# Kernel optimization log

Measured on AMD Instinct MI355X. Metric: run time of the kernel, lower is better.

## Reference

```python
import jax, jax.numpy as jnp
import numpy as np

MASK_THR = 0.2
EPS = 1e-12  # torch F.normalize eps


def setup_inputs() -> dict:
    key = jax.random.key(0)
    k1, k2, k3 = jax.random.split(key, 3)
    B, Cin, H, W = 2, 384, 96, 96
    features = jax.random.normal(k1, (B, Cin, H, W), dtype=jnp.float32)
    # projector: Conv2d(384,256,1) -> ReLU -> Conv2d(256,128,1); 1x1 convs == per-pixel GEMMs
    W1 = jax.random.normal(k2, (256, Cin), dtype=jnp.float32) * (1.0 / np.sqrt(Cin))
    b1 = jnp.zeros((256,), dtype=jnp.float32)
    W2 = jax.random.normal(k3, (128, 256), dtype=jnp.float32) * (1.0 / np.sqrt(256))
    b2 = jnp.zeros((128,), dtype=jnp.float32)
    return {"features": features, "W1": W1, "b1": b1, "W2": W2, "b2": b2}


def reference(features, W1, b1, W2, b2):
    B, _, H, Wd = features.shape
    # projector (1x1 convs as channel GEMMs)
    h = jax.nn.relu(jnp.einsum('oc,bchw->bohw', W1, features) + b1[None, :, None, None])
    feat = jnp.einsum('oc,bchw->bohw', W2, h) + b2[None, :, None, None]  # [B,128,H,W]
    # get_mask: L2-normalize over channels, full pairwise similarity, top-2 NN, distance, threshold
    norm = jnp.sqrt(jnp.sum(feat * feat, axis=1, keepdims=True))
    nf = feat / jnp.maximum(norm, EPS)
    C = nf.shape[1]
    rf = jnp.transpose(nf, (0, 2, 3, 1)).reshape(B, H * Wd, C)         # [B,N,C]
    sim = jnp.einsum('bnc,bmc->bnm', rf, rf)                           # [B,N,N]
    _, top2_idx = jax.lax.top_k(sim, 2)
    nn_idx = top2_idx[:, :, 1]                                         # nearest non-self neighbor
    nearest = jnp.take_along_axis(rf, nn_idx[:, :, None], axis=1)      # [B,N,C]
    diff = rf - nearest
    distance = jnp.sqrt(jnp.sum(diff * diff, axis=-1))                 # [B,N]
    mask = (distance > MASK_THR).astype(feat.dtype).reshape(B, 1, H, Wd)
    return mask, distance
```

## Files before the change

### kernel.cpp

```cpp
#include <hip/hip_runtime.h>

#define NHW 9216
#define NB 2
#define NCHUNK 16

typedef short s8v __attribute__((ext_vector_type(8)));
typedef _Float16 h8v __attribute__((ext_vector_type(8)));
typedef float f4v __attribute__((ext_vector_type(4)));
typedef unsigned int u32;
typedef unsigned short u16;

__device__ inline u16 f2bf(float x) {
    u32 u = __float_as_uint(x);
    u += 0x7fffu + ((u >> 16) & 1u);
    return (u16)(u >> 16);
}
__device__ inline u16 f2h(float x) {
    _Float16 h = (_Float16)x;
    return *(u16*)&h;
}

__global__ __launch_bounds__(256) void k_xsplit(const float* __restrict__ X,
                                                u16* __restrict__ xh)
{
    __shared__ float fs[64][65];
    const int tid = threadIdx.x;
    const int b = blockIdx.z, p0 = blockIdx.x * 64, half = blockIdx.y;
    const size_t fb = (size_t)b * 384 * NHW;
    const int px = tid >> 2, sub = tid & 3;
    const size_t g = (size_t)b * NHW + p0 + px;
    for (int pass = half * 3; pass < half * 3 + 3; ++pass) {
        int c0p = pass * 64;
        __syncthreads();
#pragma unroll
        for (int r = 0; r < 16; ++r) {
            int e = r * 256 + tid;
            int cc = e >> 6, p = e & 63;
            fs[cc][p] = X[fb + (size_t)(c0p + cc) * NHW + p0 + p];
        }
        __syncthreads();
        u16 hb[16];
#pragma unroll
        for (int i = 0; i < 16; ++i) hb[i] = f2h(fs[sub * 16 + i][px]);
        size_t o = g * 384 + c0p + sub * 16;
        *(s8v*)&xh[o]     = *(s8v*)&hb[0];
        *(s8v*)&xh[o + 8] = *(s8v*)&hb[8];
    }
}

__global__ __launch_bounds__(256) void k_wsplit(const float* __restrict__ W1,
                                                const float* __restrict__ W2,
                                                u16* __restrict__ w1h, u16* __restrict__ w1l,
                                                u16* __restrict__ w2h)
{
    int i = blockIdx.x * 256 + threadIdx.x;
    if (i < 98304) {
        float v = W1[i];
        _Float16 h = (_Float16)v;
        w1h[i] = *(u16*)&h;
        w1l[i] = f2h(v - (float)h);
    } else {
        int j = i - 98304;
        w2h[j] = f2h(W2[j]);
    }
}

__global__ __launch_bounds__(256, 4) void k_gemm1(const u16* __restrict__ xh,
                                                  const u16* __restrict__ w1h, const u16* __restrict__ w1l,
                                                  const float* __restrict__ b1,
                                                  u16* __restrict__ hh)
{
    union __align__(16) SM {
        struct { u16 B[2][16][512]; } stg;
        u16 bounce[128 * 66];
    };
    __shared__ SM sm;
    const int tid = threadIdx.x;
    const int wave = tid >> 6, l = tid & 63, l15 = l & 15, q = l >> 4;
    const int bx = blockIdx.x;
    const int xcd = bx & 7, k = bx >> 3;
    const int g0 = (xcd * 18 + (k >> 2)) * 128;
    const int c0 = (k & 3) * 64;
    const int gw = g0 + wave * 32;

    auto stage = [&](int kt, int buf) {
#pragma unroll
        for (int r = 0; r < 4; ++r) {
            int cid = r * 4 + wave;
            int spl = cid >> 3, kf = (cid >> 2) & 1, cs = cid & 3;
            const u16* src = (spl ? w1l : w1h) + (size_t)(c0 + cs * 16 + l15) * 384 + kt + kf * 32 + q * 8;
            __builtin_amdgcn_global_load_lds(
                (const __attribute__((address_space(1))) void*)src,
                (__attribute__((address_space(3))) void*)&sm.stg.B[buf][cid][0],
                16, 0, 0);
        }
    };

    f4v acc[2][4];
#pragma unroll
    for (int s = 0; s < 2; ++s)
#pragma unroll
        for (int c = 0; c < 4; ++c) acc[s][c] = (f4v){0.f, 0.f, 0.f, 0.f};

    stage(0, 0);
    __syncthreads();
    for (int t = 0; t < 6; ++t) {
        const int kt = t * 64;
        const int buf = t & 1;
        if (t < 5) stage(kt + 64, buf ^ 1);
        s8v ah[2][2];
#pragma unroll
        for (int s = 0; s < 2; ++s)
#pragma unroll
            for (int kf = 0; kf < 2; ++kf)
                ah[s][kf] = *(const s8v*)&xh[(size_t)(gw + s * 16 + l15) * 384 + kt + kf * 32 + q * 8];
#pragma unroll
        for (int kf = 0; kf < 2; ++kf)
#pragma unroll
            for (int cs = 0; cs < 4; ++cs) {
                s8v bh = *(const s8v*)&sm.stg.B[buf][kf * 4 + cs][l * 8];
                s8v bl = *(const s8v*)&sm.stg.B[buf][8 + kf * 4 + cs][l * 8];
#pragma unroll
                for (int s = 0; s < 2; ++s) {
                    acc[s][cs] = __builtin_amdgcn_mfma_f32_16x16x32_f16(*(h8v*)&ah[s][kf], *(h8v*)&bh, acc[s][cs], 0, 0, 0);
                    acc[s][cs] = __builtin_amdgcn_mfma_f32_16x16x32_f16(*(h8v*)&ah[s][kf], *(h8v*)&bl, acc[s][cs], 0, 0, 0);
                }
            }
        __syncthreads();
    }

#pragma unroll
    for (int s = 0; s < 2; ++s)
#pragma unroll
        for (int cs = 0; cs < 4; ++cs) {
            int c = cs * 16 + l15;
            float bv = b1[c0 + c];
#pragma unroll
            for (int r = 0; r < 4; ++r) {
                int px = wave * 32 + s * 16 + q * 4 + r;
                sm.bounce[px * 66 + c] = f2h(fmaxf(acc[s][cs][r] + bv, 0.f));
            }
        }
    __syncthreads();
    {
        int px = tid >> 1, half = tid & 1;
        u32 tmp[16];
#pragma unroll
        for (int j = 0; j < 16; ++j)
            tmp[j] = *(const u32*)&sm.bounce[px * 66 + half * 32 + j * 2];
        size_t o = (size_t)(g0 + px) * 256 + c0 + half * 32;
#pragma unroll
        for (int j = 0; j < 4; ++j)
            *(s8v*)&hh[o + j * 8] = ((s8v*)tmp)[j];
    }
}

__global__ __launch_bounds__(256) void k_gemm2n(const u16* __restrict__ hh,
                                                const u16* __restrict__ w2h,
                                                const float* __restrict__ b2,
                                                float* __restrict__ rf,
                                                u16* __restrict__ hib)
{
    __shared__ u16 Bs[64][512];
    const int tid = threadIdx.x;
    const int wave = tid >> 6, l = tid & 63, l15 = l & 15, q = l >> 4;
    const int bx = blockIdx.x;
    const int xcd = bx & 7, k = bx >> 3;
    const int g0 = (xcd * 36 + k) * 64;

#pragma unroll
    for (int r = 0; r < 16; ++r) {
        int cid = r * 4 + wave;
        int kf = cid >> 3, cst = cid & 7;
        const u16* src = w2h + (size_t)(cst * 16 + l15) * 256 + kf * 32 + q * 8;
        __builtin_amdgcn_global_load_lds(
            (const __attribute__((address_space(1))) void*)src,
            (__attribute__((address_space(3))) void*)&Bs[cid][0],
            16, 0, 0);
    }
    __syncthreads();

    const int gw = g0 + wave * 16;
    f4v acc[8];
#pragma unroll
    for (int c = 0; c < 8; ++c) acc[c] = (f4v){0.f, 0.f, 0.f, 0.f};

#pragma unroll
    for (int kf = 0; kf < 8; ++kf) {
        s8v ah = *(const s8v*)&hh[(size_t)(gw + l15) * 256 + kf * 32 + q * 8];
#pragma unroll
        for (int cst = 0; cst < 8; ++cst) {
            s8v bh = *(const s8v*)&Bs[kf * 8 + cst][l * 8];
            acc[cst] = __builtin_amdgcn_mfma_f32_16x16x32_f16(*(h8v*)&ah, *(h8v*)&bh, acc[cst], 0, 0, 0);
        }
    }

    float ssq[4] = {0.f, 0.f, 0.f, 0.f};
#pragma unroll
    for (int cst = 0; cst < 8; ++cst) {
        float bv = b2[cst * 16 + l15];
#pragma unroll
        for (int r = 0; r < 4; ++r) {
            acc[cst][r] += bv;
            ssq[r] += acc[cst][r] * acc[cst][r];
        }
    }
#pragma unroll
    for (int r = 0; r < 4; ++r) {
        ssq[r] += __shfl_xor(ssq[r], 1, 64);
        ssq[r] += __shfl_xor(ssq[r], 2, 64);
        ssq[r] += __shfl_xor(ssq[r], 4, 64);
        ssq[r] += __shfl_xor(ssq[r], 8, 64);
        ssq[r] = 1.0f / fmaxf(sqrtf(ssq[r]), 1e-12f);
    }
#pragma unroll
    for (int cst = 0; cst < 8; ++cst)
#pragma unroll
        for (int r = 0; r < 4; ++r) {
            float val = acc[cst][r] * ssq[r];
            size_t o = (size_t)(gw + q * 4 + r) * 128 + cst * 16 + l15;
            rf[o]  = val;
            hib[o] = f2bf(val);
        }
}

__global__ __launch_bounds__(256, 3) void k_simtop(const u16* __restrict__ hi,
                                                   int* __restrict__ cidx)
{
    __shared__ u16 Bs[2][16][512];
    const int tid  = threadIdx.x;
    const int wave = tid >> 6, l = tid & 63, l15 = l & 15, q = l >> 4;
    const int b     = blockIdx.z;
    const int rbase = blockIdx.x * 192;
    const int chunk = blockIdx.y;
    const int cbase = chunk * 576;
    const size_t base = (size_t)b * NHW;
    const int wr0 = rbase + wave * 48;

    s8v ah[3][4];
#pragma unroll
    for (int s = 0; s < 3; ++s) {
        int row = wr0 + s * 16 + l15;
#pragma unroll
        for (int kf = 0; kf < 4; ++kf)
            ah[s][kf] = *(const s8v*)&hi[(base + row) * 128 + kf * 32 + q * 8];
    }

    auto stage = [&](int colt, int buf) {
#pragma unroll
        for (int r = 0; r < 4; ++r) {
            int cid = r * 4 + wave;
            int kf = cid >> 2, cs = cid & 3;
            int col = colt + cs * 16 + l15;
            const u16* src = hi + (base + col) * 128 + kf * 32 + q * 8;
            __builtin_amdgcn_global_load_lds(
                (const __attribute__((address_space(1))) void*)src,
                (__attribute__((address_space(3))) void*)&Bs[buf][cid][0],
                16, 0, 0);
        }
    };

    u32 bk[3][4];
#pragma unroll
    for (int s = 0; s < 3; ++s)
#pragma unroll
        for (int r = 0; r < 4; ++r) bk[s][r] = 0u;

    stage(cbase, 0);
    __syncthreads();

    for (int ct = 0; ct < 9; ++ct) {
        const int colt = cbase + ct * 64;
        const int buf  = ct & 1;
        if (ct < 8) stage(colt + 64, buf ^ 1);

        f4v acc[3][4];
#pragma unroll
        for (int s = 0; s < 3; ++s)
#pragma unroll
            for (int c = 0; c < 4; ++c) acc[s][c] = (f4v){2.f, 2.f, 2.f, 2.f};

#pragma unroll
        for (int kf = 0; kf < 4; ++kf)
#pragma unroll
            for (int cs = 0; cs < 4; ++cs) {
                s8v bh = *(const s8v*)&Bs[buf][kf * 4 + cs][l * 8];
#pragma unroll
                for (int s = 0; s < 3; ++s)
                    acc[s][cs] = __builtin_amdgcn_mfma_f32_16x16x32_bf16(ah[s][kf], bh, acc[s][cs], 0, 0, 0);
            }

        const u32 tagv = (u32)(ct << 2);
        const bool hasdiag = (colt < wr0 + 48) && (wr0 < colt + 64);
        if (hasdiag) {
#pragma unroll
            for (int s = 0; s < 3; ++s)
#pragma unroll
                for (int r = 0; r < 4; ++r) {
                    const int rr = wr0 + s * 16 + q * 4 + r;
                    u32 km = 0u;
#pragma unroll
                    for (int cs = 0; cs < 4; ++cs) {
                        u32 kk = (__float_as_uint(acc[s][cs][r]) & 0xffffffc0u) | (tagv | (u32)cs);
                        if (colt + cs * 16 + l15 == rr) kk = 0u;
                        km = kk > km ? kk : km;
                    }
                    bk[s][r] = km > bk[s][r] ? km : bk[s][r];
                }
        } else {
#pragma unroll
            for (int s = 0; s < 3; ++s)
#pragma unroll
                for (int r = 0; r < 4; ++r) {
                    u32 km = 0u;
#pragma unroll
                    for (int cs = 0; cs < 4; ++cs) {
                        u32 kk = (__float_as_uint(acc[s][cs][r]) & 0xffffffc0u) | (tagv | (u32)cs);
                        km = kk > km ? kk : km;
                    }
                    bk[s][r] = km > bk[s][r] ? km : bk[s][r];
                }
        }
        __syncthreads();
    }

#pragma unroll
    for (int s = 0; s < 3; ++s)
#pragma unroll
        for (int r = 0; r < 4; ++r) {
            u32 key = bk[s][r];
            float v = __uint_as_float(key & 0xffffffc0u);
            int ctw = (int)((key >> 2) & 15u);
            int csw = (int)(key & 3u);
            int col = cbase + ctw * 64 + csw * 16 + l15;
#pragma unroll
            for (int d = 1; d < 16; d <<= 1) {
                float ov = __shfl_xor(v, d, 64);
                int   oi = __shfl_xor(col, d, 64);
                bool p = (ov > v) || (ov == v && oi < col);
                v   = p ? ov : v;
                col = p ? oi : col;
            }
            if (l15 == 0) {
                int row = wr0 + s * 16 + q * 4 + r;
                cidx[(base + row) * NCHUNK + chunk] = col;
            }
        }
}

__global__ __launch_bounds__(256) void k_finish(const float* __restrict__ rf,
                                                const int* __restrict__ cidx,
                                                float* __restrict__ out)
{
    const int tid = threadIdx.x;
    const int g = blockIdx.x * 16 + (tid >> 4);
    const int l15 = tid & 15;
    const int b = g / NHW;
    const size_t rowbase = (size_t)b * NHW;

    const float* x = rf + (size_t)g * 128;
    f4v x0 = *(const f4v*)&x[l15 * 8];
    f4v x1 = *(const f4v*)&x[l15 * 8 + 4];

    float bestS = -2.f; int bestI = 0;
#pragma unroll
    for (int j = 0; j < NCHUNK; ++j) {
        int c = cidx[(size_t)g * NCHUNK + j];
        const float* y = rf + (rowbase + c) * 128;
        f4v y0 = *(const f4v*)&y[l15 * 8];
        f4v y1 = *(const f4v*)&y[l15 * 8 + 4];
        float s = x0[0]*y0[0] + x0[1]*y0[1] + x0[2]*y0[2] + x0[3]*y0[3]
                + x1[0]*y1[0] + x1[1]*y1[1] + x1[2]*y1[2] + x1[3]*y1[3];
#pragma unroll
        for (int d = 1; d < 16; d <<= 1) s += __shfl_xor(s, d, 64);
        bool p = (s > bestS) || (s == bestS && c < bestI);
        bestS = p ? s : bestS;
        bestI = p ? c : bestI;
    }

    const float* y = rf + (rowbase + bestI) * 128;
    f4v y0 = *(const f4v*)&y[l15 * 8];
    f4v y1 = *(const f4v*)&y[l15 * 8 + 4];
    float d0 = x0[0]-y0[0], d1 = x0[1]-y0[1], d2 = x0[2]-y0[2], d3 = x0[3]-y0[3];
    float e0 = x1[0]-y1[0], e1 = x1[1]-y1[1], e2 = x1[2]-y1[2], e3 = x1[3]-y1[3];
    float ss = d0*d0 + d1*d1 + d2*d2 + d3*d3 + e0*e0 + e1*e1 + e2*e2 + e3*e3;
#pragma unroll
    for (int d = 1; d < 16; d <<= 1) ss += __shfl_xor(ss, d, 64);
    if (l15 == 0) {
        float dist = sqrtf(ss);
        out[NB * NHW + g] = dist;
        out[g] = dist > 0.2f ? 1.0f : 0.0f;
    }
}

extern "C" void kernel_launch(void* const* d_in, const int* in_sizes, int n_in,
                              void* d_out, int out_size, void* d_ws, size_t ws_size,
                              hipStream_t stream) {
    const float* features = (const float*)d_in[0];
    const float* W1 = (const float*)d_in[1];
    const float* b1 = (const float*)d_in[2];
    const float* W2 = (const float*)d_in[3];
    const float* b2 = (const float*)d_in[4];
    float* out = (float*)d_out;
    float* ws  = (float*)d_ws;

    u16*   xh   = (u16*)ws;
    u16*   hh   = (u16*)(ws + 3538944);
    u16*   w1h  = (u16*)(ws + 5898240);
    u16*   w1l  = (u16*)(ws + 5947392);
    u16*   w2h  = (u16*)(ws + 5996544);
    float* rf   = ws;
    u16*   hib  = (u16*)(ws + 2359296);
    int*   cidx = (int*)(ws + 3538944);

    k_xsplit<<<dim3(144, 2, NB), 256, 0, stream>>>(features, xh);
    k_wsplit<<<512, 256, 0, stream>>>(W1, W2, w1h, w1l, w2h);
    k_gemm1<<<576, 256, 0, stream>>>(xh, w1h, w1l, b1, hh);
    k_gemm2n<<<288, 256, 0, stream>>>(hh, w2h, b2, rf, hib);
    k_simtop<<<dim3(48, NCHUNK, NB), 256, 0, stream>>>(hib, cidx);
    k_finish<<<1152, 256, 0, stream>>>(rf, cidx, out);
}
```

Measured before the change: 187.0 us.

## Quantize normalized features to int8 and use i8 MFMA for similarity top-k

The similarity search now quantizes the L2-normalized features to int8 (scale 181) instead of bf16 and computes the pairwise dot products with the int8 16x16x64 MFMA, accumulating in int32. Integer scores are packed into the argmax key with a bias. Each block also grows from 192 to 256 rows, with four 16-row strips per wave, and launch bounds change to 2 blocks per SM. The aim is to double MFMA throughput and halve the operand bytes moved. The coarser quantization risks picking a different nearest neighbor when similarities are close, although the final distance is still computed from the fp32 features.

```diff
diff --git a/kernel.cpp b/kernel.cpp
--- a/kernel.cpp
+++ b/kernel.cpp
@@ -7,14 +7,13 @@
 typedef short s8v __attribute__((ext_vector_type(8)));
 typedef _Float16 h8v __attribute__((ext_vector_type(8)));
 typedef float f4v __attribute__((ext_vector_type(4)));
+typedef int i4v __attribute__((ext_vector_type(4)));
 typedef unsigned int u32;
 typedef unsigned short u16;
 
-__device__ inline u16 f2bf(float x) {
-    u32 u = __float_as_uint(x);
-    u += 0x7fffu + ((u >> 16) & 1u);
-    return (u16)(u >> 16);
-}
+#define QSCALE 181.0f
+#define IBIAS  2097152
+
 __device__ inline u16 f2h(float x) {
     _Float16 h = (_Float16)x;
     return *(u16*)&h;
@@ -159,7 +158,7 @@
                                                 const u16* __restrict__ w2h,
                                                 const float* __restrict__ b2,
                                                 float* __restrict__ rf,
-                                                u16* __restrict__ hib)
+                                                signed char* __restrict__ qi8)
 {
     __shared__ u16 Bs[64][512];
     const int tid = threadIdx.x;
@@ -219,40 +218,41 @@
         for (int r = 0; r < 4; ++r) {
             float val = acc[cst][r] * ssq[r];
             size_t o = (size_t)(gw + q * 4 + r) * 128 + cst * 16 + l15;
-            rf[o]  = val;
-            hib[o] = f2bf(val);
-        }
-}
-
-__global__ __launch_bounds__(256, 3) void k_simtop(const u16* __restrict__ hi,
+            rf[o] = val;
+            int qv = __float2int_rn(fminf(fmaxf(val * QSCALE, -127.f), 127.f));
+            qi8[o] = (signed char)qv;
+        }
+}
+
+__global__ __launch_bounds__(256, 2) void k_simtop(const signed char* __restrict__ qi,
                                                    int* __restrict__ cidx)
 {
-    __shared__ u16 Bs[2][16][512];
+    __shared__ signed char Bs[2][8][1024];
     const int tid  = threadIdx.x;
     const int wave = tid >> 6, l = tid & 63, l15 = l & 15, q = l >> 4;
     const int b     = blockIdx.z;
-    const int rbase = blockIdx.x * 192;
+    const int rbase = blockIdx.x * 256;
     const int chunk = blockIdx.y;
     const int cbase = chunk * 576;
     const size_t base = (size_t)b * NHW;
-    const int wr0 = rbase + wave * 48;
-
-    s8v ah[3][4];
-#pragma unroll
-    for (int s = 0; s < 3; ++s) {
+    const int wr0 = rbase + wave * 64;
+
+    i4v ah[4][2];
+#pragma unroll
+    for (int s = 0; s < 4; ++s) {
         int row = wr0 + s * 16 + l15;
 #pragma unroll
-        for (int kf = 0; kf < 4; ++kf)
-            ah[s][kf] = *(const s8v*)&hi[(base + row) * 128 + kf * 32 + q * 8];
+        for (int kf = 0; kf < 2; ++kf)
+            ah[s][kf] = *(const i4v*)&qi[(base + row) * 128 + kf * 64 + q * 16];
     }
 
     auto stage = [&](int colt, int buf) {
 #pragma unroll
-        for (int r = 0; r < 4; ++r) {
+        for (int r = 0; r < 2; ++r) {
             int cid = r * 4 + wave;
             int kf = cid >> 2, cs = cid & 3;
             int col = colt + cs * 16 + l15;
-            const u16* src = hi + (base + col) * 128 + kf * 32 + q * 8;
+            const signed char* src = qi + (base + col) * 128 + kf * 64 + q * 16;
             __builtin_amdgcn_global_load_lds(
                 (const __attribute__((address_space(1))) void*)src,
                 (__attribute__((address_space(3))) void*)&Bs[buf][cid][0],
@@ -260,9 +260,9 @@
         }
     };
 
-    u32 bk[3][4];
-#pragma unroll
-    for (int s = 0; s < 3; ++s)
+    u32 bk[4][4];
+#pragma unroll
+    for (int s = 0; s < 4; ++s)
 #pragma unroll
         for (int r = 0; r < 4; ++r) bk[s][r] = 0u;
 
@@ -274,34 +274,34 @@
         const int buf  = ct & 1;
         if (ct < 8) stage(colt + 64, buf ^ 1);
 
-        f4v acc[3][4];
-#pragma unroll
-        for (int s = 0; s < 3; ++s)
-#pragma unroll
-            for (int c = 0; c < 4; ++c) acc[s][c] = (f4v){2.f, 2.f, 2.f, 2.f};
-
-#pragma unroll
-        for (int kf = 0; kf < 4; ++kf)
+        i4v acc[4][4];
+#pragma unroll
+        for (int s = 0; s < 4; ++s)
+#pragma unroll
+            for (int c = 0; c < 4; ++c) acc[s][c] = (i4v){IBIAS, IBIAS, IBIAS, IBIAS};
+
+#pragma unroll
+        for (int kf = 0; kf < 2; ++kf)
 #pragma unroll
             for (int cs = 0; cs < 4; ++cs) {
-                s8v bh = *(const s8v*)&Bs[buf][kf * 4 + cs][l * 8];
-#pragma unroll
-                for (int s = 0; s < 3; ++s)
-                    acc[s][cs] = __builtin_amdgcn_mfma_f32_16x16x32_bf16(ah[s][kf], bh, acc[s][cs], 0, 0, 0);
+                i4v bh = *(const i4v*)&Bs[buf][kf * 4 + cs][l * 16];
+#pragma unroll
+                for (int s = 0; s < 4; ++s)
+                    acc[s][cs] = __builtin_amdgcn_mfma_i32_16x16x64_i8(ah[s][kf], bh, acc[s][cs], 0, 0, 0);
             }
 
         const u32 tagv = (u32)(ct << 2);
-        const bool hasdiag = (colt < wr0 + 48) && (wr0 < colt + 64);
+        const bool hasdiag = (colt < wr0 + 64) && (wr0 < colt + 64);
         if (hasdiag) {
 #pragma unroll
-            for (int s = 0; s < 3; ++s)
+            for (int s = 0; s < 4; ++s)
 #pragma unroll
                 for (int r = 0; r < 4; ++r) {
                     const int rr = wr0 + s * 16 + q * 4 + r;
                     u32 km = 0u;
 #pragma unroll
                     for (int cs = 0; cs < 4; ++cs) {
-                        u32 kk = (__float_as_uint(acc[s][cs][r]) & 0xffffffc0u) | (tagv | (u32)cs);
+                        u32 kk = ((u32)acc[s][cs][r] << 6) | (tagv | (u32)cs);
                         if (colt + cs * 16 + l15 == rr) kk = 0u;
                         km = kk > km ? kk : km;
                     }
@@ -309,13 +309,13 @@
                 }
         } else {
 #pragma unroll
-            for (int s = 0; s < 3; ++s)
+            for (int s = 0; s < 4; ++s)
 #pragma unroll
                 for (int r = 0; r < 4; ++r) {
                     u32 km = 0u;
 #pragma unroll
                     for (int cs = 0; cs < 4; ++cs) {
-                        u32 kk = (__float_as_uint(acc[s][cs][r]) & 0xffffffc0u) | (tagv | (u32)cs);
+                        u32 kk = ((u32)acc[s][cs][r] << 6) | (tagv | (u32)cs);
                         km = kk > km ? kk : km;
                     }
                     bk[s][r] = km > bk[s][r] ? km : bk[s][r];
@@ -325,20 +325,20 @@
     }
 
 #pragma unroll
-    for (int s = 0; s < 3; ++s)
+    for (int s = 0; s < 4; ++s)
 #pragma unroll
         for (int r = 0; r < 4; ++r) {
             u32 key = bk[s][r];
-            float v = __uint_as_float(key & 0xffffffc0u);
+            int sv = (int)(key >> 6);
             int ctw = (int)((key >> 2) & 15u);
             int csw = (int)(key & 3u);
             int col = cbase + ctw * 64 + csw * 16 + l15;
 #pragma unroll
             for (int d = 1; d < 16; d <<= 1) {
-                float ov = __shfl_xor(v, d, 64);
-                int   oi = __shfl_xor(col, d, 64);
-                bool p = (ov > v) || (ov == v && oi < col);
-                v   = p ? ov : v;
+                int ov = __shfl_xor(sv, d, 64);
+                int oi = __shfl_xor(col, d, 64);
+                bool p = (ov > sv) || (ov == sv && oi < col);
+                sv  = p ? ov : sv;
                 col = p ? oi : col;
             }
             if (l15 == 0) {
@@ -410,13 +410,13 @@
     u16*   w1l  = (u16*)(ws + 5947392);
     u16*   w2h  = (u16*)(ws + 5996544);
     float* rf   = ws;
-    u16*   hib  = (u16*)(ws + 2359296);
+    signed char* qi8 = (signed char*)(ws + 2359296);
     int*   cidx = (int*)(ws + 3538944);
 
     k_xsplit<<<dim3(144, 2, NB), 256, 0, stream>>>(features, xh);
     k_wsplit<<<512, 256, 0, stream>>>(W1, W2, w1h, w1l, w2h);
     k_gemm1<<<576, 256, 0, stream>>>(xh, w1h, w1l, b1, hh);
-    k_gemm2n<<<288, 256, 0, stream>>>(hh, w2h, b2, rf, hib);
-    k_simtop<<<dim3(48, NCHUNK, NB), 256, 0, stream>>>(hib, cidx);
+    k_gemm2n<<<288, 256, 0, stream>>>(hh, w2h, b2, rf, qi8);
+    k_simtop<<<dim3(36, NCHUNK, NB), 256, 0, stream>>>(qi8, cidx);
     k_finish<<<1152, 256, 0, stream>>>(rf, cidx, out);
 }
```

New measurement: 164.4 us. 12.1% less time.
